# Kernel optimization log

Measured on AMD Instinct MI355X. Metric: run time of the kernel, lower is better.

Reference implementation:

```python
import jax, jax.numpy as jnp
import numpy as np

MARGIN = 50.0

def setup_inputs() -> dict:
    key = jax.random.key(0)
    k1, k2 = jax.random.split(key)
    N, D = 4096, 768
    rep_anchor = jax.random.normal(k1, (N, D), dtype=jnp.float32)
    rep_pos = jax.random.normal(k2, (N, D), dtype=jnp.float32)
    return {"rep_anchor": rep_anchor, "rep_pos": rep_pos}

def reference(rep_anchor, rep_pos):
    # pairwise euclidean distances: dist[i, j] = ||anchor_i - pos_j||_2
    # (F.pairwise_distance with p=2, eps handled implicitly; use stable sqrt)
    a2 = jnp.sum(rep_anchor * rep_anchor, axis=1, keepdims=True)   # [N,1]
    p2 = jnp.sum(rep_pos * rep_pos, axis=1, keepdims=True).T       # [1,N]
    cross = rep_anchor @ rep_pos.T                                  # [N,N]
    sq = jnp.maximum(a2 + p2 - 2.0 * cross, 0.0)
    dist = jnp.sqrt(sq + 1e-12)
    scores = MARGIN - dist                                          # [N,N]
    # row-wise negative log-softmax, take diagonal (positive pair at index i)
    logp = jax.nn.log_softmax(scores, axis=1)
    loss_per_row = -jnp.diagonal(logp)                               # [N]
    return loss_per_row.mean()
```

## Files before the change

kernel.cpp:

```cpp
#include <hip/hip_runtime.h>
#include <hip/hip_bf16.h>
#include <stdint.h>


#define N_ROWS 4096
#define D_DIM  768
#define GRID_DIM (N_ROWS / 128)
#define NITER (D_DIM / 64)

typedef float f32x4 __attribute__((ext_vector_type(4)));
typedef short bf16x8 __attribute__((ext_vector_type(8)));

struct bh4 { __hip_bfloat16 a, b, c, d; };

__global__ __launch_bounds__(256) void cvt_norms(
        const float* __restrict__ A, const float* __restrict__ P,
        __hip_bfloat16* __restrict__ Ab, __hip_bfloat16* __restrict__ Pb,
        float* __restrict__ a2, float* __restrict__ p2, float* __restrict__ S) {
    const int t = threadIdx.x, lane = t & 63, wave = t >> 6;
    const int row = blockIdx.x * 4 + wave;
    const float* src = blockIdx.y ? P : A;
    __hip_bfloat16* dst = blockIdx.y ? Pb : Ab;
    float* nrm = blockIdx.y ? p2 : a2;

    const float4* s4 = (const float4*)src + (size_t)row * (D_DIM / 4);
    bh4* d4 = (bh4*)dst + (size_t)row * (D_DIM / 4);
    float s = 0.0f;
#pragma unroll
    for (int c = 0; c < 3; c++) {
        float4 v = s4[c * 64 + lane];
        s += v.x * v.x + v.y * v.y + v.z * v.z + v.w * v.w;
        bh4 o;
        o.a = __float2bfloat16(v.x); o.b = __float2bfloat16(v.y);
        o.c = __float2bfloat16(v.z); o.d = __float2bfloat16(v.w);
        d4[c * 64 + lane] = o;
    }
    for (int off = 32; off; off >>= 1) s += __shfl_down(s, off);
    if (lane == 0) {
        nrm[row] = s;
        if (blockIdx.y == 0) S[row] = 0.0f;
    }
}

__device__ __forceinline__ void g2l16(const void* g, void* l) {
    __builtin_amdgcn_global_load_lds(
        (const __attribute__((address_space(1))) void*)g,
        (__attribute__((address_space(3))) void*)l, 16, 0, 0);
}

__global__ __launch_bounds__(256) void gemm_fused(
        const __hip_bfloat16* __restrict__ Ab, const __hip_bfloat16* __restrict__ Pb,
        const float* __restrict__ a2, const float* __restrict__ p2,
        float* __restrict__ S, float* __restrict__ Dd) {
    __shared__ __align__(16) unsigned short As[2][128 * 64];
    __shared__ __align__(16) unsigned short Bs[2][128 * 64];

    const int bm = blockIdx.x, bn = blockIdx.y;
    const int t = threadIdx.x;
    const int lane = t & 63, wave = t >> 6;
    const int wm = wave >> 1, wn = wave & 1;

    f32x4 acc[4][4];
#pragma unroll
    for (int i = 0; i < 4; i++)
#pragma unroll
        for (int j = 0; j < 4; j++) acc[i][j] = (f32x4){0.f, 0.f, 0.f, 0.f};

    const int rT = t >> 3;
    const int sg = (t & 7) ^ (rT & 7);
    const size_t aBase = (size_t)(bm * 128 + rT) * D_DIM + sg * 8;
    const size_t bBase = (size_t)(bn * 128 + rT) * D_DIM + sg * 8;

    const int fr = lane & 15, fq = lane >> 4;
    const int xr = fr & 7;
    const int aRow = (wm * 64 + fr) * 64;
    const int bRow = (wn * 64 + fr) * 64;

#define STAGE(K2, SEL)                                                          \
    do {                                                                        \
        const int k0_ = (K2) * 64;                                              \
        _Pragma("unroll")                                                       \
        for (int c = 0; c < 4; c++)                                             \
            g2l16(Ab + aBase + c * (32 * D_DIM) + k0_, &As[SEL][(c * 256 + t) * 8]); \
        _Pragma("unroll")                                                       \
        for (int c = 0; c < 4; c++)                                             \
            g2l16(Pb + bBase + c * (32 * D_DIM) + k0_, &Bs[SEL][(c * 256 + t) * 8]); \
    } while (0)

    STAGE(0, 0);

    for (int k = 0; k < NITER; k++) {
        const int cur = k & 1;
        asm volatile("s_waitcnt vmcnt(0)" ::: "memory");
        asm volatile("s_barrier" ::: "memory");
        if (k + 1 < NITER) STAGE(k + 1, cur ^ 1);

#pragma unroll
        for (int tt = 0; tt < 2; tt++) {
            const int vA = (((tt << 2) | fq) ^ xr) * 8;
            bf16x8 af[4], bfr[4];
#pragma unroll
            for (int mi = 0; mi < 4; mi++)
                af[mi] = *(const bf16x8*)(As[cur] + aRow + mi * 1024 + vA);
#pragma unroll
            for (int ni = 0; ni < 4; ni++)
                bfr[ni] = *(const bf16x8*)(Bs[cur] + bRow + ni * 1024 + vA);
#pragma unroll
            for (int mi = 0; mi < 4; mi++)
#pragma unroll
                for (int ni = 0; ni < 4; ni++)
                    acc[mi][ni] = __builtin_amdgcn_mfma_f32_16x16x32_bf16(
                        af[mi], bfr[ni], acc[mi][ni], 0, 0, 0);
        }
    }
#undef STAGE

    float p2v[4];
#pragma unroll
    for (int ni = 0; ni < 4; ni++)
        p2v[ni] = p2[bn * 128 + wn * 64 + ni * 16 + (lane & 15)];
    const int colBase = bn * 128 + wn * 64 + (lane & 15);

#pragma unroll
    for (int mi = 0; mi < 4; mi++) {
#pragma unroll
        for (int r = 0; r < 4; r++) {
            const int gi = bm * 128 + wm * 64 + mi * 16 + (lane >> 4) * 4 + r;
            const float a2v = a2[gi];
            float rs = 0.0f;
#pragma unroll
            for (int ni = 0; ni < 4; ni++) {
                const float cross = acc[mi][ni][r];
                const float sq = a2v + p2v[ni] - 2.0f * cross;
                const float dist = sqrtf(fmaxf(sq, 0.0f) + 1e-12f);
                const int gj = colBase + ni * 16;
                if (gi == gj) Dd[gi] = dist;
                rs += __expf(-dist);
            }
            rs += __shfl_xor(rs, 1);
            rs += __shfl_xor(rs, 2);
            rs += __shfl_xor(rs, 4);
            rs += __shfl_xor(rs, 8);
            if ((lane & 15) == 0) atomicAdd(&S[gi], rs);
        }
    }
}

__global__ void finalize(const float* __restrict__ S, const float* __restrict__ Dd,
                         float* __restrict__ out) {
    const int t = threadIdx.x;
    float s = 0.0f;
    for (int i = t; i < N_ROWS; i += 256) s += Dd[i] + logf(S[i]);
    for (int off = 32; off; off >>= 1) s += __shfl_down(s, off);
    __shared__ float wsum[4];
    if ((t & 63) == 0) wsum[t >> 6] = s;
    __syncthreads();
    if (t == 0) out[0] = (wsum[0] + wsum[1] + wsum[2] + wsum[3]) * (1.0f / N_ROWS);
}

__global__ void zero_out1(float* __restrict__ out) {
    if (threadIdx.x == 0 && blockIdx.x == 0) out[0] = 0.0f;
}
__global__ void naive_row(const float* __restrict__ A, const float* __restrict__ P,
                          float* __restrict__ out) {
    __shared__ float arow[D_DIM];
    const int i = blockIdx.x, t = threadIdx.x;
    for (int c = t; c < D_DIM; c += 256) arow[c] = A[(size_t)i * D_DIM + c];
    __syncthreads();
    float sumexp = 0.0f, ddiag = 0.0f;
    for (int j = t; j < N_ROWS; j += 256) {
        const float* p = P + (size_t)j * D_DIM;
        float d2 = 0.0f;
        for (int c = 0; c < D_DIM; c++) { float df = arow[c] - p[c]; d2 += df * df; }
        float dist = sqrtf(fmaxf(d2, 0.0f) + 1e-12f);
        if (j == i) ddiag = dist;
        sumexp += __expf(-dist);
    }
    for (int off = 32; off; off >>= 1) {
        sumexp += __shfl_down(sumexp, off);
        ddiag  += __shfl_down(ddiag, off);
    }
    __shared__ float w1[4], w2[4];
    if ((t & 63) == 0) { w1[t >> 6] = sumexp; w2[t >> 6] = ddiag; }
    __syncthreads();
    if (t == 0) {
        float se = w1[0] + w1[1] + w1[2] + w1[3];
        float dd = w2[0] + w2[1] + w2[2] + w2[3];
        atomicAdd(out, (dd + logf(se)) * (1.0f / N_ROWS));
    }
}

extern "C" void kernel_launch(void* const* d_in, const int* in_sizes, int n_in,
                              void* d_out, int out_size, void* d_ws, size_t ws_size,
                              hipStream_t stream) {
    const float* A = (const float*)d_in[0];
    const float* P = (const float*)d_in[1];
    float* out = (float*)d_out;

    const size_t BF_BYTES = (size_t)N_ROWS * D_DIM * sizeof(__hip_bfloat16);
    const size_t V_BYTES  = (size_t)N_ROWS * sizeof(float);
    const size_t NEED = 2 * BF_BYTES + 4 * V_BYTES;

    if (ws_size >= NEED) {
        char* ws = (char*)d_ws;
        __hip_bfloat16* Ab = (__hip_bfloat16*)(ws);
        __hip_bfloat16* Pb = (__hip_bfloat16*)(ws + BF_BYTES);
        float* a2 = (float*)(ws + 2 * BF_BYTES);
        float* p2 = (float*)(ws + 2 * BF_BYTES + V_BYTES);
        float* S  = (float*)(ws + 2 * BF_BYTES + 2 * V_BYTES);
        float* Dd = (float*)(ws + 2 * BF_BYTES + 3 * V_BYTES);

        hipLaunchKernelGGL(cvt_norms, dim3(N_ROWS / 4, 2), dim3(256), 0, stream,
                           A, P, Ab, Pb, a2, p2, S);
        hipLaunchKernelGGL(gemm_fused, dim3(GRID_DIM, GRID_DIM), dim3(256), 0, stream,
                           Ab, Pb, a2, p2, S, Dd);
        hipLaunchKernelGGL(finalize, dim3(1), dim3(256), 0, stream, S, Dd, out);
    } else {
        hipLaunchKernelGGL(zero_out1, dim3(1), dim3(64), 0, stream, out);
        hipLaunchKernelGGL(naive_row, dim3(N_ROWS), dim3(256), 0, stream, A, P, out);
    }
}
```

Before: 122.5 us.

## Switch cross-product GEMM from bf16 to fp8 e4m3 with scaled MFMA

After: 142.5 us. 16.3% more time.

```diff
diff --git a/kernel.cpp b/kernel.cpp
--- a/kernel.cpp
+++ b/kernel.cpp
@@ -1,39 +1,41 @@
 #include <hip/hip_runtime.h>
 #include <hip/hip_bf16.h>
+#include <hip/hip_fp8.h>
 #include <stdint.h>
 
 
 #define N_ROWS 4096
 #define D_DIM  768
 #define GRID_DIM (N_ROWS / 128)
-#define NITER (D_DIM / 64)
+#define NITER (D_DIM / 128)
 
 typedef float f32x4 __attribute__((ext_vector_type(4)));
-typedef short bf16x8 __attribute__((ext_vector_type(8)));
-
-struct bh4 { __hip_bfloat16 a, b, c, d; };
+typedef int   i32x4 __attribute__((ext_vector_type(4)));
+typedef int   i32x8 __attribute__((ext_vector_type(8)));
 
 __global__ __launch_bounds__(256) void cvt_norms(
         const float* __restrict__ A, const float* __restrict__ P,
-        __hip_bfloat16* __restrict__ Ab, __hip_bfloat16* __restrict__ Pb,
+        uint8_t* __restrict__ A8, uint8_t* __restrict__ P8,
         float* __restrict__ a2, float* __restrict__ p2, float* __restrict__ S) {
     const int t = threadIdx.x, lane = t & 63, wave = t >> 6;
     const int row = blockIdx.x * 4 + wave;
     const float* src = blockIdx.y ? P : A;
-    __hip_bfloat16* dst = blockIdx.y ? Pb : Ab;
+    uint8_t* dst = blockIdx.y ? P8 : A8;
     float* nrm = blockIdx.y ? p2 : a2;
 
     const float4* s4 = (const float4*)src + (size_t)row * (D_DIM / 4);
-    bh4* d4 = (bh4*)dst + (size_t)row * (D_DIM / 4);
+    uint32_t* d4 = (uint32_t*)dst + (size_t)row * (D_DIM / 4);
     float s = 0.0f;
 #pragma unroll
     for (int c = 0; c < 3; c++) {
         float4 v = s4[c * 64 + lane];
         s += v.x * v.x + v.y * v.y + v.z * v.z + v.w * v.w;
-        bh4 o;
-        o.a = __float2bfloat16(v.x); o.b = __float2bfloat16(v.y);
-        o.c = __float2bfloat16(v.z); o.d = __float2bfloat16(v.w);
-        d4[c * 64 + lane] = o;
+        union { uint32_t u; uint8_t b[4]; } pk;
+        pk.b[0] = __hip_fp8_e4m3(v.x).__x;
+        pk.b[1] = __hip_fp8_e4m3(v.y).__x;
+        pk.b[2] = __hip_fp8_e4m3(v.z).__x;
+        pk.b[3] = __hip_fp8_e4m3(v.w).__x;
+        d4[c * 64 + lane] = pk.u;
     }
     for (int off = 32; off; off >>= 1) s += __shfl_down(s, off);
     if (lane == 0) {
@@ -49,11 +51,11 @@
 }
 
 __global__ __launch_bounds__(256) void gemm_fused(
-        const __hip_bfloat16* __restrict__ Ab, const __hip_bfloat16* __restrict__ Pb,
+        const uint8_t* __restrict__ A8, const uint8_t* __restrict__ P8,
         const float* __restrict__ a2, const float* __restrict__ p2,
         float* __restrict__ S, float* __restrict__ Dd) {
-    __shared__ __align__(16) unsigned short As[2][128 * 64];
-    __shared__ __align__(16) unsigned short Bs[2][128 * 64];
+    __shared__ __align__(16) uint8_t As[2][128 * 128];
+    __shared__ __align__(16) uint8_t Bs[2][128 * 128];
 
     const int bm = blockIdx.x, bn = blockIdx.y;
     const int t = threadIdx.x;
@@ -68,23 +70,25 @@
 
     const int rT = t >> 3;
     const int sg = (t & 7) ^ (rT & 7);
-    const size_t aBase = (size_t)(bm * 128 + rT) * D_DIM + sg * 8;
-    const size_t bBase = (size_t)(bn * 128 + rT) * D_DIM + sg * 8;
+    const size_t aBase = (size_t)(bm * 128 + rT) * D_DIM + (size_t)sg * 16;
+    const size_t bBase = (size_t)(bn * 128 + rT) * D_DIM + (size_t)sg * 16;
 
     const int fr = lane & 15, fq = lane >> 4;
     const int xr = fr & 7;
-    const int aRow = (wm * 64 + fr) * 64;
-    const int bRow = (wn * 64 + fr) * 64;
-
-#define STAGE(K2, SEL)                                                          \
-    do {                                                                        \
-        const int k0_ = (K2) * 64;                                              \
-        _Pragma("unroll")                                                       \
-        for (int c = 0; c < 4; c++)                                             \
-            g2l16(Ab + aBase + c * (32 * D_DIM) + k0_, &As[SEL][(c * 256 + t) * 8]); \
-        _Pragma("unroll")                                                       \
-        for (int c = 0; c < 4; c++)                                             \
-            g2l16(Pb + bBase + c * (32 * D_DIM) + k0_, &Bs[SEL][(c * 256 + t) * 8]); \
+    const int aRow = (wm * 64 + fr) * 128;
+    const int bRow = (wn * 64 + fr) * 128;
+    const int c0 = ((2 * fq + 0) ^ xr) * 16;
+    const int c1 = ((2 * fq + 1) ^ xr) * 16;
+
+#define STAGE(K2, SEL)                                                             \
+    do {                                                                           \
+        const int k0_ = (K2) * 128;                                                \
+        _Pragma("unroll")                                                          \
+        for (int c = 0; c < 4; c++)                                                \
+            g2l16(A8 + aBase + c * (32 * D_DIM) + k0_, &As[SEL][(c * 256 + t) * 16]); \
+        _Pragma("unroll")                                                          \
+        for (int c = 0; c < 4; c++)                                                \
+            g2l16(P8 + bBase + c * (32 * D_DIM) + k0_, &Bs[SEL][(c * 256 + t) * 16]); \
     } while (0)
 
     STAGE(0, 0);
@@ -95,23 +99,28 @@
         asm volatile("s_barrier" ::: "memory");
         if (k + 1 < NITER) STAGE(k + 1, cur ^ 1);
 
-#pragma unroll
-        for (int tt = 0; tt < 2; tt++) {
-            const int vA = (((tt << 2) | fq) ^ xr) * 8;
-            bf16x8 af[4], bfr[4];
-#pragma unroll
-            for (int mi = 0; mi < 4; mi++)
-                af[mi] = *(const bf16x8*)(As[cur] + aRow + mi * 1024 + vA);
+        i32x8 af[4], bfr[4];
+#pragma unroll
+        for (int mi = 0; mi < 4; mi++) {
+            i32x4 lo = *(const i32x4*)&As[cur][aRow + mi * (16 * 128) + c0];
+            i32x4 hi = *(const i32x4*)&As[cur][aRow + mi * (16 * 128) + c1];
+            af[mi] = __builtin_shufflevector(lo, hi, 0, 1, 2, 3, 4, 5, 6, 7);
+        }
+#pragma unroll
+        for (int ni = 0; ni < 4; ni++) {
+            i32x4 lo = *(const i32x4*)&Bs[cur][bRow + ni * (16 * 128) + c0];
+            i32x4 hi = *(const i32x4*)&Bs[cur][bRow + ni * (16 * 128) + c1];
+            bfr[ni] = __builtin_shufflevector(lo, hi, 0, 1, 2, 3, 4, 5, 6, 7);
+        }
+#pragma unroll
+        for (int mi = 0; mi < 4; mi++)
 #pragma unroll
             for (int ni = 0; ni < 4; ni++)
-                bfr[ni] = *(const bf16x8*)(Bs[cur] + bRow + ni * 1024 + vA);
-#pragma unroll
-            for (int mi = 0; mi < 4; mi++)
-#pragma unroll
-                for (int ni = 0; ni < 4; ni++)
-                    acc[mi][ni] = __builtin_amdgcn_mfma_f32_16x16x32_bf16(
-                        af[mi], bfr[ni], acc[mi][ni], 0, 0, 0);
-        }
+                acc[mi][ni] = __builtin_amdgcn_mfma_scale_f32_16x16x128_f8f6f4(
+                    af[mi], bfr[ni], acc[mi][ni],
+                    0, 0,
+                    0, 0x7F7F7F7F,
+                    0, 0x7F7F7F7F);
     }
 #undef STAGE
 
@@ -197,23 +206,23 @@
     const float* P = (const float*)d_in[1];
     float* out = (float*)d_out;
 
-    const size_t BF_BYTES = (size_t)N_ROWS * D_DIM * sizeof(__hip_bfloat16);
+    const size_t F8_BYTES = (size_t)N_ROWS * D_DIM;
     const size_t V_BYTES  = (size_t)N_ROWS * sizeof(float);
-    const size_t NEED = 2 * BF_BYTES + 4 * V_BYTES;
+    const size_t NEED = 2 * F8_BYTES + 4 * V_BYTES;
 
     if (ws_size >= NEED) {
         char* ws = (char*)d_ws;
-        __hip_bfloat16* Ab = (__hip_bfloat16*)(ws);
-        __hip_bfloat16* Pb = (__hip_bfloat16*)(ws + BF_BYTES);
-        float* a2 = (float*)(ws + 2 * BF_BYTES);
-        float* p2 = (float*)(ws + 2 * BF_BYTES + V_BYTES);
-        float* S  = (float*)(ws + 2 * BF_BYTES + 2 * V_BYTES);
-        float* Dd = (float*)(ws + 2 * BF_BYTES + 3 * V_BYTES);
+        uint8_t* A8 = (uint8_t*)(ws);
+        uint8_t* P8 = (uint8_t*)(ws + F8_BYTES);
+        float* a2 = (float*)(ws + 2 * F8_BYTES);
+        float* p2 = (float*)(ws + 2 * F8_BYTES + V_BYTES);
+        float* S  = (float*)(ws + 2 * F8_BYTES + 2 * V_BYTES);
+        float* Dd = (float*)(ws + 2 * F8_BYTES + 3 * V_BYTES);
 
         hipLaunchKernelGGL(cvt_norms, dim3(N_ROWS / 4, 2), dim3(256), 0, stream,
-                           A, P, Ab, Pb, a2, p2, S);
+                           A, P, A8, P8, a2, p2, S);
         hipLaunchKernelGGL(gemm_fused, dim3(GRID_DIM, GRID_DIM), dim3(256), 0, stream,
-                           Ab, Pb, a2, p2, S, Dd);
+                           A8, P8, a2, p2, S, Dd);
         hipLaunchKernelGGL(finalize, dim3(1), dim3(256), 0, stream, S, Dd, out);
     } else {
         hipLaunchKernelGGL(zero_out1, dim3(1), dim3(64), 0, stream, out);
```
